# Kernel optimization log

Hardware: AMD Instinct MI355X
Metric: run time of the kernel (lower is better)

The kernel has to match this reference:

```python
import jax, jax.numpy as jnp
import numpy as np

NUM_HEADS = 16
BLOCK_SIZE = 64
NUM_GLOBAL_TOKENS = 64
WINDOW_SIZE = 256
NUM_RANDOM_BLOCKS = 3
BATCH = 2
SEQ_LEN = 4096
EMBED_DIM = 1024


def _alibi_slopes(n):
    # power-of-2 head count path of _compute_alibi_slopes
    base = 2.0 ** (-(2.0 ** (-(np.log2(n) - 3.0))))
    return jnp.asarray([base ** i for i in range(1, n + 1)], dtype=jnp.float32)


def _build_block_indices():
    nb = SEQ_LEN // BLOCK_SIZE
    ngb = NUM_GLOBAL_TOKENS // BLOCK_SIZE
    wb = WINDOW_SIZE // BLOCK_SIZE
    mb = 2 * wb + 1 + NUM_RANDOM_BLOCKS
    rng = np.random.default_rng(0)
    out = np.full((nb, mb), -1, dtype=np.int64)
    for qb in range(nb):
        attended = set(range(ngb))  # global blocks handled separately
        idx = 0
        for kb in range(max(ngb, qb - wb), min(nb, qb + wb + 1)):
            if kb not in attended:
                out[qb, idx] = kb
                attended.add(kb)
                idx += 1
        cand = [b for b in range(ngb, nb) if b not in attended]
        pick = rng.choice(len(cand), size=min(NUM_RANDOM_BLOCKS, len(cand)), replace=False)
        for j in pick:
            out[qb, idx] = cand[j]
            idx += 1
    return jnp.asarray(out)


def setup_inputs() -> dict:
    key = jax.random.key(0)
    ks = jax.random.split(key, 5)
    s = 0.02
    x = jax.random.normal(ks[0], (BATCH, SEQ_LEN, EMBED_DIM), jnp.float32)
    Wq = jax.random.normal(ks[1], (EMBED_DIM, EMBED_DIM), jnp.float32) * s
    Wk = jax.random.normal(ks[2], (EMBED_DIM, EMBED_DIM), jnp.float32) * s
    Wv = jax.random.normal(ks[3], (EMBED_DIM, EMBED_DIM), jnp.float32) * s
    Wo = jax.random.normal(ks[4], (EMBED_DIM, EMBED_DIM), jnp.float32) * s
    return {"x": x, "Wq": Wq, "Wk": Wk, "Wv": Wv, "Wo": Wo,
            "block_indices": _build_block_indices()}


def reference(x, Wq, Wk, Wv, Wo, block_indices):
    B, S, E = x.shape
    H = NUM_HEADS
    Dh = E // H
    G = NUM_GLOBAL_TOKENS
    BS = BLOCK_SIZE
    scale = 1.0 / np.sqrt(Dh)

    def split_heads(t):
        return t.reshape(B, S, H, Dh).transpose(0, 2, 1, 3)  # [B,H,S,Dh]

    q = split_heads(x @ Wq)
    k = split_heads(x @ Wk)
    v = split_heads(x @ Wv)

    slopes = _alibi_slopes(H)  # [H]
    pos = jnp.arange(S, dtype=jnp.float32)

    # ---- global tokens: full attention over all keys ----
    sg = jnp.einsum('bhgd,bhsd->bhgs', q[:, :, :G], k) * scale
    bias_g = -slopes[:, None, None] * jnp.abs(pos[:G, None] - pos[None, :])  # [H,G,S]
    pg = jax.nn.softmax(sg + bias_g[None], axis=-1)
    out_g = jnp.einsum('bhgs,bhsd->bhgd', pg, v)  # [B,H,G,Dh]

    # ---- sparse queries: global KV + gathered sparse blocks ----
    nb = S // BS
    ngb = G // BS
    nqb = nb - ngb
    bi = block_indices[ngb:]           # [nqb, MB], -1 = padding
    mb = bi.shape[1]
    bsafe = jnp.maximum(bi, 0)

    kb = k.reshape(B, H, nb, BS, Dh)
    vb = v.reshape(B, H, nb, BS, Dh)
    kg = kb[:, :, bsafe].reshape(B, H, nqb, mb * BS, Dh)
    vg = vb[:, :, bsafe].reshape(B, H, nqb, mb * BS, Dh)
    kglob = jnp.broadcast_to(k[:, :, None, :G], (B, H, nqb, G, Dh))
    vglob = jnp.broadcast_to(v[:, :, None, :G], (B, H, nqb, G, Dh))
    kcat = jnp.concatenate([kglob, kg], axis=3)  # [B,H,nqb,G+mb*BS,Dh]
    vcat = jnp.concatenate([vglob, vg], axis=3)

    qn = q[:, :, G:].reshape(B, H, nqb, BS, Dh)
    scores = jnp.einsum('bhqmd,bhqnd->bhqmn', qn, kcat) * scale

    qpos = (G + jnp.arange(nqb * BS, dtype=jnp.float32)).reshape(nqb, BS)
    loc_pos = (bsafe[:, :, None] * BS + jnp.arange(BS)[None, None, :]).reshape(nqb, mb * BS).astype(jnp.float32)
    kpos = jnp.concatenate([jnp.broadcast_to(pos[:G][None], (nqb, G)), loc_pos], axis=1)
    bias = -slopes[:, None, None, None] * jnp.abs(qpos[None, :, :, None] - kpos[None, :, None, :])  # [H,nqb,BS,Kt]

    valid = jnp.concatenate([jnp.ones((nqb, G), bool), jnp.repeat(bi >= 0, BS, axis=1)], axis=1)
    scores = jnp.where(valid[None, None, :, None, :], scores + bias[None], -jnp.inf)
    p = jax.nn.softmax(scores, axis=-1)
    out_s = jnp.einsum('bhqmn,bhqnd->bhqmd', p, vcat).reshape(B, H, S - G, Dh)

    out = jnp.concatenate([out_g, out_s], axis=2)  # [B,H,S,Dh]
    out = out.transpose(0, 2, 1, 3).reshape(B, S, E)
    return out @ Wo
```

## Files before the change

kernel.cpp:

```cpp
#include <hip/hip_runtime.h>
#include <stdint.h>

typedef __attribute__((ext_vector_type(8))) short short8;
typedef __attribute__((ext_vector_type(4))) float f32x4;
typedef __attribute__((ext_vector_type(8))) unsigned short u16x8;
typedef __attribute__((ext_vector_type(2))) unsigned int u32x2;

#define DEV static __device__ __forceinline__

DEV unsigned short f2bf(float f) {
  union { float f; uint32_t u; } v; v.f = f;
  uint32_t r = v.u + 0x7FFFu + ((v.u >> 16) & 1u);
  return (unsigned short)(r >> 16);
}

DEV void gload16(const void* g, void* l) {
  __builtin_amdgcn_global_load_lds(
      (const __attribute__((address_space(1))) void*)g,
      (__attribute__((address_space(3))) void*)l, 16, 0, 0);
}

__global__ void cast_x_kernel(const float* __restrict__ x, unsigned short* __restrict__ xb) {
  int i = blockIdx.x * 256 + threadIdx.x;
  f32x4 a = ((const f32x4*)x)[2 * i];
  f32x4 b = ((const f32x4*)x)[2 * i + 1];
  u16x8 o;
  o[0] = f2bf(a[0]); o[1] = f2bf(a[1]); o[2] = f2bf(a[2]); o[3] = f2bf(a[3]);
  o[4] = f2bf(b[0]); o[5] = f2bf(b[1]); o[6] = f2bf(b[2]); o[7] = f2bf(b[3]);
  ((u16x8*)xb)[i] = o;
}

__global__ void transpose_w_kernel(const float* __restrict__ Wq, const float* __restrict__ Wk,
                                   const float* __restrict__ Wv, const float* __restrict__ Wo,
                                   unsigned short* __restrict__ wt) {
  __shared__ float tile[64][65];
  int z = blockIdx.z;
  const float* W = (z == 0) ? Wq : (z == 1) ? Wk : (z == 2) ? Wv : Wo;
  unsigned short* dst = wt + (size_t)z * 1024 * 1024;
  int bn = blockIdx.x, bk = blockIdx.y;
  int t = threadIdx.x;
  int c = t & 63, rr = t >> 6;
#pragma unroll
  for (int p = 0; p < 16; ++p) {
    int r = p * 4 + rr;
    tile[r][c] = W[(size_t)(bk * 64 + r) * 1024 + bn * 64 + c];
  }
  __syncthreads();
#pragma unroll
  for (int p = 0; p < 16; ++p) {
    int r2 = p * 4 + rr;
    dst[(size_t)(bn * 64 + r2) * 1024 + bk * 64 + c] = f2bf(tile[c][r2]);
  }
}

__global__ __launch_bounds__(256, 2) void gemm_qkv(const unsigned short* __restrict__ A,
                                                   const unsigned short* __restrict__ wt,
                                                   unsigned short* __restrict__ Qb,
                                                   unsigned short* __restrict__ Kb,
                                                   unsigned short* __restrict__ Vtb,
                                                   float qscale) {
  constexpr int K = 1024;
  __shared__ __align__(16) unsigned short As[2][128 * 64];
  __shared__ __align__(16) unsigned short Bs[2][128 * 64];
  int flat = blockIdx.x + 24 * blockIdx.y;
  int xcd = flat & 7, idx = flat >> 3;
  int bm = xcd * 8 + (idx & 7);
  int bn = idx >> 3;
  int which = bn >> 3, bnn = bn & 7;
  int tid = threadIdx.x, lane = tid & 63, w = tid >> 6;
  int wr = w >> 1, wc = w & 1;
  f32x4 acc[4][4] = {};

  int sr[4], soff[4];
#pragma unroll
  for (int i = 0; i < 4; ++i) {
    int ci = w * 4 + i;
    int r = ci * 8 + (lane >> 3);
    sr[i] = r;
    soff[i] = ((lane & 7) ^ (r & 7)) * 8;
  }
  const unsigned short* Arow = A + (size_t)(bm * 128) * K;
  const unsigned short* Brow = wt + (size_t)which * 1048576 + (size_t)(bnn * 128) * K;

  auto STAGE = [&](int bi, int k0) {
#pragma unroll
    for (int i = 0; i < 4; ++i) {
      gload16(Arow + (size_t)sr[i] * K + k0 + soff[i], &As[bi][(w * 4 + i) * 512]);
      gload16(Brow + (size_t)sr[i] * K + k0 + soff[i], &Bs[bi][(w * 4 + i) * 512]);
    }
  };

  STAGE(0, 0);
  for (int kt = 0; kt < 16; ++kt) {
    int cur = kt & 1;
    if (kt < 15) {
      STAGE(cur ^ 1, (kt + 1) * 64);
      asm volatile("s_waitcnt vmcnt(8)" ::: "memory");
    } else {
      asm volatile("s_waitcnt vmcnt(0)" ::: "memory");
    }
    __builtin_amdgcn_s_barrier();
    __builtin_amdgcn_sched_barrier(0);
    short8 af[2][4], bfr[2][4];
#pragma unroll
    for (int c = 0; c < 2; ++c) {
#pragma unroll
      for (int m = 0; m < 4; ++m) {
        int cc = (lane >> 4) + 4 * c;
        int ra = wr * 64 + m * 16 + (lane & 15);
        af[c][m] = *(const short8*)(&As[cur][ra * 64 + ((cc ^ (ra & 7)) * 8)]);
        int rb = wc * 64 + m * 16 + (lane & 15);
        bfr[c][m] = *(const short8*)(&Bs[cur][rb * 64 + ((cc ^ (rb & 7)) * 8)]);
      }
    }
#pragma unroll
    for (int c = 0; c < 2; ++c)
#pragma unroll
      for (int m = 0; m < 4; ++m)
#pragma unroll
        for (int n = 0; n < 4; ++n)
          acc[m][n] = __builtin_amdgcn_mfma_f32_16x16x32_bf16(af[c][m], bfr[c][n], acc[m][n], 0, 0, 0);
    __builtin_amdgcn_s_barrier();
    __builtin_amdgcn_sched_barrier(0);
  }

  int rbase = bm * 128 + wr * 64;
  int cbase = bnn * 128 + wc * 64;
#pragma unroll
  for (int m = 0; m < 4; ++m)
#pragma unroll
    for (int n = 0; n < 4; ++n) {
      int row0 = rbase + m * 16 + (lane >> 4) * 4;
      int col = cbase + n * 16 + (lane & 15);
      int h = col >> 6, d = col & 63;
      int b = row0 >> 12, s0 = row0 & 4095;
      if (which == 0) {
#pragma unroll
        for (int reg = 0; reg < 4; ++reg)
          Qb[((size_t)(b * 16 + h) * 4096 + s0 + reg) * 64 + d] = f2bf(acc[m][n][reg] * qscale);
      } else if (which == 1) {
#pragma unroll
        for (int reg = 0; reg < 4; ++reg)
          Kb[((size_t)(b * 16 + h) * 4096 + s0 + reg) * 64 + d] = f2bf(acc[m][n][reg]);
      } else {
        u32x2 pk;
        asm("v_cvt_pk_bf16_f32 %0, %1, %2" : "=v"(pk[0]) : "v"(acc[m][n][0]), "v"(acc[m][n][1]));
        asm("v_cvt_pk_bf16_f32 %0, %1, %2" : "=v"(pk[1]) : "v"(acc[m][n][2]), "v"(acc[m][n][3]));
        *(u32x2*)(Vtb + ((((size_t)(b * 16 + h) * 64 + (s0 >> 6)) * 64 + d) * 64 + (s0 & 63))) = pk;
      }
    }
}

__global__ __launch_bounds__(256, 2) void gemm_out(const unsigned short* __restrict__ A,
                                                   const unsigned short* __restrict__ Bt,
                                                   float* __restrict__ dst) {
  constexpr int K = 1024;
  __shared__ __align__(16) unsigned short As[2][128 * 64];
  __shared__ __align__(16) unsigned short Bs[2][128 * 64];
  int flat = blockIdx.x + 8 * blockIdx.y;
  int xcd = flat & 7, idx = flat >> 3;
  int bm = xcd * 8 + (idx & 7);
  int bn = idx >> 3;
  int tid = threadIdx.x, lane = tid & 63, w = tid >> 6;
  int wr = w >> 1, wc = w & 1;
  f32x4 acc[4][4] = {};

  int sr[4], soff[4];
#pragma unroll
  for (int i = 0; i < 4; ++i) {
    int ci = w * 4 + i;
    int r = ci * 8 + (lane >> 3);
    sr[i] = r;
    soff[i] = ((lane & 7) ^ (r & 7)) * 8;
  }
  const unsigned short* Arow = A + (size_t)(bm * 128) * K;
  const unsigned short* Brow = Bt + (size_t)(bn * 128) * K;

  auto STAGE = [&](int bi, int k0) {
#pragma unroll
    for (int i = 0; i < 4; ++i) {
      gload16(Arow + (size_t)sr[i] * K + k0 + soff[i], &As[bi][(w * 4 + i) * 512]);
      gload16(Brow + (size_t)sr[i] * K + k0 + soff[i], &Bs[bi][(w * 4 + i) * 512]);
    }
  };

  STAGE(0, 0);
  for (int kt = 0; kt < 16; ++kt) {
    int cur = kt & 1;
    if (kt < 15) {
      STAGE(cur ^ 1, (kt + 1) * 64);
      asm volatile("s_waitcnt vmcnt(8)" ::: "memory");
    } else {
      asm volatile("s_waitcnt vmcnt(0)" ::: "memory");
    }
    __builtin_amdgcn_s_barrier();
    __builtin_amdgcn_sched_barrier(0);
    short8 af[2][4], bfr[2][4];
#pragma unroll
    for (int c = 0; c < 2; ++c) {
#pragma unroll
      for (int m = 0; m < 4; ++m) {
        int cc = (lane >> 4) + 4 * c;
        int ra = wr * 64 + m * 16 + (lane & 15);
        af[c][m] = *(const short8*)(&As[cur][ra * 64 + ((cc ^ (ra & 7)) * 8)]);
        int rb = wc * 64 + m * 16 + (lane & 15);
        bfr[c][m] = *(const short8*)(&Bs[cur][rb * 64 + ((cc ^ (rb & 7)) * 8)]);
      }
    }
#pragma unroll
    for (int c = 0; c < 2; ++c)
#pragma unroll
      for (int m = 0; m < 4; ++m)
#pragma unroll
        for (int n = 0; n < 4; ++n)
          acc[m][n] = __builtin_amdgcn_mfma_f32_16x16x32_bf16(af[c][m], bfr[c][n], acc[m][n], 0, 0, 0);
    __builtin_amdgcn_s_barrier();
    __builtin_amdgcn_sched_barrier(0);
  }

  int rbase = bm * 128 + wr * 64;
  int cbase = bn * 128 + wc * 64;
#pragma unroll
  for (int m = 0; m < 4; ++m)
#pragma unroll
    for (int n = 0; n < 4; ++n) {
      int row0 = rbase + m * 16 + (lane >> 4) * 4;
      int col = cbase + n * 16 + (lane & 15);
#pragma unroll
      for (int reg = 0; reg < 4; ++reg)
        dst[(size_t)(row0 + reg) * 1024 + col] = acc[m][n][reg];
    }
}

__global__ __launch_bounds__(256) void attn_kernel(const unsigned short* __restrict__ Qh,
                            const unsigned short* __restrict__ Kh,
                            const unsigned short* __restrict__ Vbt,
                            const int* __restrict__ bidx,
                            unsigned short* __restrict__ attn_out,
                            float* __restrict__ Opart,
                            float* __restrict__ lpart) {
  __shared__ __align__(16) unsigned short Ks[3][64 * 64];
  __shared__ __align__(16) unsigned short Vs[3][64 * 64];
  int flat = blockIdx.x + 71 * blockIdx.y;
  int nf = (flat & 7) * 284 + (flat >> 3);
  int gx = nf % 71, bh = nf / 71;
  int h = bh & 15;
  int tid = threadIdx.x, lane = tid & 63, w = tid >> 6;
  int q = lane & 15, g = lane >> 4;
  float slope2 = exp2f(-0.5f * (float)(h + 1)) * 1.44269504f;

  int qb, nkb;
  int vlist;
  if (gx < 63) {
    qb = gx + 1;
    int v = -1;
    if (lane == 0) v = 0;
    else if (lane <= 12) v = bidx[qb * 12 + (lane - 1)];
    vlist = v;
    unsigned long long msk = __ballot(v >= 0);
    nkb = __builtin_popcountll(msk & 0x1FFFull);
  } else {
    qb = 0;
    nkb = 8;
    vlist = (gx - 63) * 8 + lane;
  }

  int qrow = qb * 64 + w * 16 + q;
  const unsigned short* qptr = Qh + ((size_t)bh * 4096 + qrow) * 64 + g * 8;
  short8 qf0 = *(const short8*)qptr;
  short8 qf1 = *(const short8*)(qptr + 32);

  float qposf = (float)qrow;
  float sq = slope2 * qposf;
  float er[4][4];
#pragma unroll
  for (int ct = 0; ct < 4; ++ct)
#pragma unroll
    for (int r = 0; r < 4; ++r) er[ct][r] = slope2 * (float)(ct * 16 + r);

  float psum = 0.f;
  f32x4 accO[4] = {};

  const unsigned short* Kbh = Kh + (size_t)bh * 4096 * 64;
  const unsigned short* Vbh = Vbt + (size_t)bh * 4096 * 64;

  int srr[2], so[2];
#pragma unroll
  for (int i = 0; i < 2; ++i) {
    int ci = w * 2 + i;
    int r = ci * 8 + (lane >> 3);
    srr[i] = r;
    so[i] = ((lane & 7) ^ (r & 7)) * 8;
  }
  auto STAGE = [&](int bi, int kb) {
    const unsigned short* kbase = Kbh + (size_t)kb * 4096;
    const unsigned short* vbase = Vbh + (size_t)kb * 4096;
#pragma unroll
    for (int i = 0; i < 2; ++i) {
      gload16(kbase + srr[i] * 64 + so[i], &Ks[bi][(w * 2 + i) * 512]);
      gload16(vbase + srr[i] * 64 + so[i], &Vs[bi][(w * 2 + i) * 512]);
    }
  };

  STAGE(0, __builtin_amdgcn_readlane(vlist, 0));
  STAGE(1, __builtin_amdgcn_readlane(vlist, 1));

  for (int it = 0; it < nkb; ++it) {
    int cur = it % 3;
    int kb = __builtin_amdgcn_readlane(vlist, it);
    if (it + 1 < nkb) {
      asm volatile("s_waitcnt vmcnt(4)" ::: "memory");
    } else {
      asm volatile("s_waitcnt vmcnt(0)" ::: "memory");
    }
    __builtin_amdgcn_s_barrier();
    __builtin_amdgcn_sched_barrier(0);
    if (it + 2 < nkb) STAGE((it + 2) % 3, __builtin_amdgcn_readlane(vlist, it + 2));

    float kb4g = (float)(kb * 64 + 4 * g);
    float d_[4][4];
    if (kb != qb) {
      if (kb < qb) {
        float t = __builtin_fmaf(slope2, kb4g, -sq);
#pragma unroll
        for (int ct = 0; ct < 4; ++ct)
#pragma unroll
          for (int r = 0; r < 4; ++r) d_[ct][r] = t + er[ct][r];
      } else {
        float t = sq - slope2 * kb4g;
#pragma unroll
        for (int ct = 0; ct < 4; ++ct)
#pragma unroll
          for (int r = 0; r < 4; ++r) d_[ct][r] = t - er[ct][r];
      }
    } else {
      float db = qposf - kb4g;
#pragma unroll
      for (int ct = 0; ct < 4; ++ct)
#pragma unroll
        for (int r = 0; r < 4; ++r)
          d_[ct][r] = -slope2 * fabsf(db - (float)(ct * 16 + r));
    }

    float pv[4][4];
    __builtin_amdgcn_s_setprio(1);
#pragma unroll
    for (int ct = 0; ct < 4; ++ct) {
      int kr = ct * 16 + q;
      short8 kf0 = *(const short8*)(&Ks[cur][kr * 64 + ((g ^ (kr & 7)) * 8)]);
      short8 kf1 = *(const short8*)(&Ks[cur][kr * 64 + (((g + 4) ^ (kr & 7)) * 8)]);
      f32x4 cin = {d_[ct][0], d_[ct][1], d_[ct][2], d_[ct][3]};
      f32x4 s = __builtin_amdgcn_mfma_f32_16x16x32_bf16(kf0, qf0, cin, 0, 0, 0);
      s = __builtin_amdgcn_mfma_f32_16x16x32_bf16(kf1, qf1, s, 0, 0, 0);
#pragma unroll
      for (int r = 0; r < 4; ++r) {
        float p = exp2f(s[r]);
        pv[ct][r] = p;
        psum += p;
      }
    }
    __builtin_amdgcn_s_setprio(0);

    uint32_t pkw[4][2];
#pragma unroll
    for (int ct = 0; ct < 4; ++ct) {
      asm("v_cvt_pk_bf16_f32 %0, %1, %2" : "=v"(pkw[ct][0]) : "v"(pv[ct][0]), "v"(pv[ct][1]));
      asm("v_cvt_pk_bf16_f32 %0, %1, %2" : "=v"(pkw[ct][1]) : "v"(pv[ct][2]), "v"(pv[ct][3]));
    }
    bool odd = (tid & 16) != 0;
    short8 pa[2];
#pragma unroll
    for (int f = 0; f < 2; ++f) {
      uint32_t s0 = pkw[2 * f][0], s1 = pkw[2 * f][1];
      uint32_t t0 = pkw[2 * f + 1][0], t1 = pkw[2 * f + 1][1];
      asm("v_permlane32_swap_b32 %0, %1" : "+v"(s0), "+v"(t0));
      asm("v_permlane32_swap_b32 %0, %1" : "+v"(s1), "+v"(t1));
      uint32_t xs0 = (uint32_t)__shfl_xor((int)s0, 16, 64);
      uint32_t xs1 = (uint32_t)__shfl_xor((int)s1, 16, 64);
      uint32_t xt0 = (uint32_t)__shfl_xor((int)t0, 16, 64);
      uint32_t xt1 = (uint32_t)__shfl_xor((int)t1, 16, 64);
      union { uint32_t w[4]; short8 v; } u;
      u.w[0] = odd ? xt0 : s0;
      u.w[1] = odd ? xt1 : s1;
      u.w[2] = odd ? t0 : xs0;
      u.w[3] = odd ? t1 : xs1;
      pa[f] = u.v;
    }

    __builtin_amdgcn_s_setprio(1);
#pragma unroll
    for (int dt = 0; dt < 4; ++dt) {
      int dr = dt * 16 + q;
      short8 vf0 = *(const short8*)(&Vs[cur][dr * 64 + ((g ^ (dr & 7)) * 8)]);
      short8 vf1 = *(const short8*)(&Vs[cur][dr * 64 + (((g + 4) ^ (dr & 7)) * 8)]);
      accO[dt] = __builtin_amdgcn_mfma_f32_16x16x32_bf16(pa[0], vf0, accO[dt], 0, 0, 0);
      accO[dt] = __builtin_amdgcn_mfma_f32_16x16x32_bf16(pa[1], vf1, accO[dt], 0, 0, 0);
    }
    __builtin_amdgcn_s_setprio(0);
  }

  float lt = psum;
  lt += __shfl_xor(lt, 16, 64);
  lt += __shfl_xor(lt, 32, 64);

  int b = bh >> 4;
  if (gx < 63) {
#pragma unroll
    for (int reg = 0; reg < 4; ++reg) {
      float ls = __shfl(lt, 4 * g + reg, 64);
      float rl = 1.0f / ls;
      int row = qb * 64 + w * 16 + 4 * g + reg;
#pragma unroll
      for (int dt = 0; dt < 4; ++dt) {
        int col = h * 64 + dt * 16 + q;
        attn_out[((size_t)b * 4096 + row) * 1024 + col] = f2bf(accO[dt][reg] * rl);
      }
    }
  } else {
    int chunk = gx - 63;
    float* Op = Opart + (size_t)(bh * 8 + chunk) * 64 * 64;
    float* lp = lpart + (size_t)(bh * 8 + chunk) * 64;
#pragma unroll
    for (int reg = 0; reg < 4; ++reg) {
      int row = w * 16 + 4 * g + reg;
#pragma unroll
      for (int dt = 0; dt < 4; ++dt) {
        int col = dt * 16 + q;
        Op[row * 64 + col] = accO[dt][reg];
      }
    }
    if (g == 0) lp[w * 16 + q] = lt;
  }
}

__global__ void merge_qb0(const float* __restrict__ Opart, const float* __restrict__ lpart,
                          unsigned short* __restrict__ attn_out) {
  int bh = blockIdx.x;
  int tid = threadIdx.x;
  int row = tid >> 2, cg = tid & 3;
  const float* lp = lpart + (size_t)bh * 8 * 64;
  float L = 0.f;
#pragma unroll
  for (int c = 0; c < 8; ++c) L += lp[c * 64 + row];
  float rL = 1.0f / L;
  int b = bh >> 4, h = bh & 15;
  f32x4 acc0 = {}, acc1 = {}, acc2 = {}, acc3 = {};
#pragma unroll
  for (int c = 0; c < 8; ++c) {
    const float* Op = Opart + ((size_t)(bh * 8 + c) * 64 + row) * 64 + cg * 16;
    acc0 += ((const f32x4*)Op)[0];
    acc1 += ((const f32x4*)Op)[1];
    acc2 += ((const f32x4*)Op)[2];
    acc3 += ((const f32x4*)Op)[3];
  }
  unsigned short* out = attn_out + ((size_t)b * 4096 + row) * 1024 + h * 64 + cg * 16;
#pragma unroll
  for (int j = 0; j < 4; ++j) {
    out[j] = f2bf(acc0[j] * rL);
    out[4 + j] = f2bf(acc1[j] * rL);
    out[8 + j] = f2bf(acc2[j] * rL);
    out[12 + j] = f2bf(acc3[j] * rL);
  }
}

extern "C" void kernel_launch(void* const* d_in, const int* in_sizes, int n_in,
                              void* d_out, int out_size, void* d_ws, size_t ws_size,
                              hipStream_t stream) {
  const float* x = (const float*)d_in[0];
  const float* Wq = (const float*)d_in[1];
  const float* Wk = (const float*)d_in[2];
  const float* Wv = (const float*)d_in[3];
  const float* Wo = (const float*)d_in[4];
  const int* bidx = (const int*)d_in[5];

  char* ws = (char*)d_ws;
  unsigned short* xb = (unsigned short*)(ws);
  unsigned short* wt = (unsigned short*)(ws + 16777216);
  unsigned short* Qb = (unsigned short*)(ws + 25165824);
  unsigned short* Kb = (unsigned short*)(ws + 41943040);
  unsigned short* Vtb = (unsigned short*)(ws + 58720256);
  unsigned short* attnb = (unsigned short*)(ws + 75497472);
  float* Opart = (float*)(ws);
  float* lpart = (float*)(ws + 4194304);

  cast_x_kernel<<<4096, 256, 0, stream>>>(x, xb);
  transpose_w_kernel<<<dim3(16, 16, 4), 256, 0, stream>>>(Wq, Wk, Wv, Wo, wt);
  gemm_qkv<<<dim3(24, 64), 256, 0, stream>>>(xb, wt, Qb, Kb, Vtb, 0.18033688f);
  attn_kernel<<<dim3(71, 32), 256, 0, stream>>>(Qb, Kb, Vtb, bidx, attnb, Opart, lpart);
  merge_qb0<<<32, 256, 0, stream>>>(Opart, lpart, attnb);
  gemm_out<<<dim3(8, 64), 256, 0, stream>>>(attnb, wt + 3145728, (float*)d_out);
}
```

Before: 166.5 us.

## Load GEMM B operand directly from global into registers, drop B LDS staging

Both projection GEMMs stop staging the weight (B) tile through shared memory. Each wave now reads its B fragments straight from global memory into registers every k-step, while A stays double-buffered in LDS, and the launch bound is raised to three blocks per CU. This halves LDS use and the LDS read traffic so occupancy can grow. In exchange, B is now read from global memory without any prefetch and is waited on within the same iteration, so global latency is exposed, and B rows are re-read redundantly by the two waves that share the same wc.

```diff
diff --git a/kernel.cpp b/kernel.cpp
--- a/kernel.cpp
+++ b/kernel.cpp
@@ -53,7 +53,7 @@
   }
 }
 
-__global__ __launch_bounds__(256, 2) void gemm_qkv(const unsigned short* __restrict__ A,
+__global__ __launch_bounds__(256, 3) void gemm_qkv(const unsigned short* __restrict__ A,
                                                    const unsigned short* __restrict__ wt,
                                                    unsigned short* __restrict__ Qb,
                                                    unsigned short* __restrict__ Kb,
@@ -61,7 +61,6 @@
                                                    float qscale) {
   constexpr int K = 1024;
   __shared__ __align__(16) unsigned short As[2][128 * 64];
-  __shared__ __align__(16) unsigned short Bs[2][128 * 64];
   int flat = blockIdx.x + 24 * blockIdx.y;
   int xcd = flat & 7, idx = flat >> 3;
   int bm = xcd * 8 + (idx & 7);
@@ -69,57 +68,61 @@
   int which = bn >> 3, bnn = bn & 7;
   int tid = threadIdx.x, lane = tid & 63, w = tid >> 6;
   int wr = w >> 1, wc = w & 1;
+  int g2 = lane >> 4;
   f32x4 acc[4][4] = {};
 
-  int sr[4], soff[4];
+  int srg[4], sof[4];
 #pragma unroll
   for (int i = 0; i < 4; ++i) {
     int ci = w * 4 + i;
     int r = ci * 8 + (lane >> 3);
-    sr[i] = r;
-    soff[i] = ((lane & 7) ^ (r & 7)) * 8;
+    srg[i] = r;
+    sof[i] = ((lane & 7) ^ (r & 7)) * 8;
   }
   const unsigned short* Arow = A + (size_t)(bm * 128) * K;
-  const unsigned short* Brow = wt + (size_t)which * 1048576 + (size_t)(bnn * 128) * K;
-
-  auto STAGE = [&](int bi, int k0) {
-#pragma unroll
-    for (int i = 0; i < 4; ++i) {
-      gload16(Arow + (size_t)sr[i] * K + k0 + soff[i], &As[bi][(w * 4 + i) * 512]);
-      gload16(Brow + (size_t)sr[i] * K + k0 + soff[i], &Bs[bi][(w * 4 + i) * 512]);
-    }
+  const unsigned short* BrowG = wt + (size_t)which * 1048576 + (size_t)(bnn * 128) * K;
+
+  auto STAGE_A = [&](int bi, int k0) {
+#pragma unroll
+    for (int i = 0; i < 4; ++i)
+      gload16(Arow + (size_t)srg[i] * K + k0 + sof[i], &As[bi][(w * 4 + i) * 512]);
   };
-
-  STAGE(0, 0);
+  auto LOADB = [&](short8 (&bf)[4][2], int k0) {
+#pragma unroll
+    for (int n = 0; n < 4; ++n)
+#pragma unroll
+      for (int s = 0; s < 2; ++s)
+        bf[n][s] = *(const short8*)(BrowG + (size_t)(wc * 64 + n * 16 + (lane & 15)) * K + k0 + s * 32 + g2 * 8);
+  };
+
+  STAGE_A(0, 0);
   for (int kt = 0; kt < 16; ++kt) {
     int cur = kt & 1;
+    short8 bf[4][2];
+    LOADB(bf, kt * 64);
     if (kt < 15) {
-      STAGE(cur ^ 1, (kt + 1) * 64);
+      STAGE_A(cur ^ 1, (kt + 1) * 64);
+      asm volatile("s_waitcnt vmcnt(12)" ::: "memory");
+    } else {
       asm volatile("s_waitcnt vmcnt(8)" ::: "memory");
-    } else {
-      asm volatile("s_waitcnt vmcnt(0)" ::: "memory");
     }
     __builtin_amdgcn_s_barrier();
     __builtin_amdgcn_sched_barrier(0);
-    short8 af[2][4], bfr[2][4];
-#pragma unroll
-    for (int c = 0; c < 2; ++c) {
+    short8 af[2][4];
+#pragma unroll
+    for (int s = 0; s < 2; ++s)
 #pragma unroll
       for (int m = 0; m < 4; ++m) {
-        int cc = (lane >> 4) + 4 * c;
         int ra = wr * 64 + m * 16 + (lane & 15);
-        af[c][m] = *(const short8*)(&As[cur][ra * 64 + ((cc ^ (ra & 7)) * 8)]);
-        int rb = wc * 64 + m * 16 + (lane & 15);
-        bfr[c][m] = *(const short8*)(&Bs[cur][rb * 64 + ((cc ^ (rb & 7)) * 8)]);
-      }
-    }
-#pragma unroll
-    for (int c = 0; c < 2; ++c)
+        af[s][m] = *(const short8*)(&As[cur][ra * 64 + (((g2 + 4 * s) ^ (ra & 7)) * 8)]);
+      }
+#pragma unroll
+    for (int s = 0; s < 2; ++s)
 #pragma unroll
       for (int m = 0; m < 4; ++m)
 #pragma unroll
         for (int n = 0; n < 4; ++n)
-          acc[m][n] = __builtin_amdgcn_mfma_f32_16x16x32_bf16(af[c][m], bfr[c][n], acc[m][n], 0, 0, 0);
+          acc[m][n] = __builtin_amdgcn_mfma_f32_16x16x32_bf16(af[s][m], bf[n][s], acc[m][n], 0, 0, 0);
     __builtin_amdgcn_s_barrier();
     __builtin_amdgcn_sched_barrier(0);
   }
@@ -151,69 +154,72 @@
     }
 }
 
-__global__ __launch_bounds__(256, 2) void gemm_out(const unsigned short* __restrict__ A,
+__global__ __launch_bounds__(256, 3) void gemm_out(const unsigned short* __restrict__ A,
                                                    const unsigned short* __restrict__ Bt,
                                                    float* __restrict__ dst) {
   constexpr int K = 1024;
   __shared__ __align__(16) unsigned short As[2][128 * 64];
-  __shared__ __align__(16) unsigned short Bs[2][128 * 64];
   int flat = blockIdx.x + 8 * blockIdx.y;
   int xcd = flat & 7, idx = flat >> 3;
   int bm = xcd * 8 + (idx & 7);
   int bn = idx >> 3;
   int tid = threadIdx.x, lane = tid & 63, w = tid >> 6;
   int wr = w >> 1, wc = w & 1;
+  int g2 = lane >> 4;
   f32x4 acc[4][4] = {};
 
-  int sr[4], soff[4];
+  int srg[4], sof[4];
 #pragma unroll
   for (int i = 0; i < 4; ++i) {
     int ci = w * 4 + i;
     int r = ci * 8 + (lane >> 3);
-    sr[i] = r;
-    soff[i] = ((lane & 7) ^ (r & 7)) * 8;
+    srg[i] = r;
+    sof[i] = ((lane & 7) ^ (r & 7)) * 8;
   }
   const unsigned short* Arow = A + (size_t)(bm * 128) * K;
-  const unsigned short* Brow = Bt + (size_t)(bn * 128) * K;
-
-  auto STAGE = [&](int bi, int k0) {
-#pragma unroll
-    for (int i = 0; i < 4; ++i) {
-      gload16(Arow + (size_t)sr[i] * K + k0 + soff[i], &As[bi][(w * 4 + i) * 512]);
-      gload16(Brow + (size_t)sr[i] * K + k0 + soff[i], &Bs[bi][(w * 4 + i) * 512]);
-    }
+  const unsigned short* BrowG = Bt + (size_t)(bn * 128) * K;
+
+  auto STAGE_A = [&](int bi, int k0) {
+#pragma unroll
+    for (int i = 0; i < 4; ++i)
+      gload16(Arow + (size_t)srg[i] * K + k0 + sof[i], &As[bi][(w * 4 + i) * 512]);
   };
-
-  STAGE(0, 0);
+  auto LOADB = [&](short8 (&bf)[4][2], int k0) {
+#pragma unroll
+    for (int n = 0; n < 4; ++n)
+#pragma unroll
+      for (int s = 0; s < 2; ++s)
+        bf[n][s] = *(const short8*)(BrowG + (size_t)(wc * 64 + n * 16 + (lane & 15)) * K + k0 + s * 32 + g2 * 8);
+  };
+
+  STAGE_A(0, 0);
   for (int kt = 0; kt < 16; ++kt) {
     int cur = kt & 1;
+    short8 bf[4][2];
+    LOADB(bf, kt * 64);
     if (kt < 15) {
-      STAGE(cur ^ 1, (kt + 1) * 64);
+      STAGE_A(cur ^ 1, (kt + 1) * 64);
+      asm volatile("s_waitcnt vmcnt(12)" ::: "memory");
+    } else {
       asm volatile("s_waitcnt vmcnt(8)" ::: "memory");
-    } else {
-      asm volatile("s_waitcnt vmcnt(0)" ::: "memory");
     }
     __builtin_amdgcn_s_barrier();
     __builtin_amdgcn_sched_barrier(0);
-    short8 af[2][4], bfr[2][4];
-#pragma unroll
-    for (int c = 0; c < 2; ++c) {
+    short8 af[2][4];
+#pragma unroll
+    for (int s = 0; s < 2; ++s)
 #pragma unroll
       for (int m = 0; m < 4; ++m) {
-        int cc = (lane >> 4) + 4 * c;
         int ra = wr * 64 + m * 16 + (lane & 15);
-        af[c][m] = *(const short8*)(&As[cur][ra * 64 + ((cc ^ (ra & 7)) * 8)]);
-        int rb = wc * 64 + m * 16 + (lane & 15);
-        bfr[c][m] = *(const short8*)(&Bs[cur][rb * 64 + ((cc ^ (rb & 7)) * 8)]);
-      }
-    }
-#pragma unroll
-    for (int c = 0; c < 2; ++c)
+        af[s][m] = *(const short8*)(&As[cur][ra * 64 + (((g2 + 4 * s) ^ (ra & 7)) * 8)]);
+      }
+#pragma unroll
+    for (int s = 0; s < 2; ++s)
 #pragma unroll
       for (int m = 0; m < 4; ++m)
 #pragma unroll
         for (int n = 0; n < 4; ++n)
-          acc[m][n] = __builtin_amdgcn_mfma_f32_16x16x32_bf16(af[c][m], bfr[c][n], acc[m][n], 0, 0, 0);
+          acc[m][n] = __builtin_amdgcn_mfma_f32_16x16x32_bf16(af[s][m], bf[n][s], acc[m][n], 0, 0, 0);
     __builtin_amdgcn_s_barrier();
     __builtin_amdgcn_sched_barrier(0);
   }
```

Measured after the change: 233.8 us. 1.4x slower.
